# Kernel optimization log

Measured on AMD Instinct MI355X. Metric: run time of the kernel, lower is better.

The kernel has to match this reference:

```python
import jax, jax.numpy as jnp
import numpy as np

B, S, D, H = 4, 4096, 512, 2
PD = D // H  # projection_dim = 256


def setup_inputs() -> dict:
    key = jax.random.key(0)
    ks = jax.random.split(key, 6)
    scale = 1.0 / np.sqrt(D)
    return {
        "x": jax.random.normal(ks[0], (B, S, D), dtype=jnp.float32),
        "Wq": jax.random.normal(ks[1], (D, D), dtype=jnp.float32) * scale,
        "bq": jnp.zeros((D,), dtype=jnp.float32),
        "Wk": jax.random.normal(ks[2], (D, D), dtype=jnp.float32) * scale,
        "bk": jnp.zeros((D,), dtype=jnp.float32),
        "Wv": jax.random.normal(ks[3], (D, D), dtype=jnp.float32) * scale,
        "bv": jnp.zeros((D,), dtype=jnp.float32),
        "Wo": jax.random.normal(ks[4], (D, D), dtype=jnp.float32) * scale,
        "bo": jnp.zeros((D,), dtype=jnp.float32),
    }


def _split_heads(t):
    # [B, S, D] -> [B, H, S, PD]
    return t.reshape(B, S, H, PD).transpose(0, 2, 1, 3)


def reference(x, Wq, bq, Wk, bk, Wv, bv, Wo, bo):
    Q = _split_heads(x @ Wq + bq)
    K = _split_heads(x @ Wk + bk)
    V = _split_heads(x @ Wv + bv)
    # scaled dot-product attention, non-causal (no mask in original)
    scores = jnp.einsum("bhqd,bhkd->bhqk", Q, K) / jnp.sqrt(jnp.float32(PD))
    weights = jax.nn.softmax(scores, axis=-1)
    attn = jnp.einsum("bhqk,bhkd->bhqd", weights, V)
    # merge heads: [B, H, S, PD] -> [B, S, D]
    concat = attn.transpose(0, 2, 1, 3).reshape(B, S, D)
    return concat @ Wo + bo
```

## Files before the change

### kernel.cpp

```cpp
#include <hip/hip_runtime.h>
#include <hip/hip_bf16.h>


#define B_  4
#define S_  4096
#define D_  512
#define H_  2
#define PD_ 256

typedef __attribute__((ext_vector_type(4))) float f32x4;
typedef __attribute__((ext_vector_type(16))) float f32x16;
typedef __attribute__((ext_vector_type(8))) short short8;
typedef __attribute__((ext_vector_type(4))) short short4v;
typedef __attribute__((ext_vector_type(4))) unsigned u32x4;

static __device__ __forceinline__ short f2bf(float f) {
  unsigned u = __float_as_uint(f);
  u += 0x7fffu + ((u >> 16) & 1u);
  return (short)(u >> 16);
}
static __device__ __forceinline__ unsigned pack2(float a, float b) {
  return (unsigned)(unsigned short)f2bf(a) | ((unsigned)(unsigned short)f2bf(b) << 16);
}
static __device__ __forceinline__ void gload16(const short* g, short* l) {
  __builtin_amdgcn_global_load_lds((const __attribute__((address_space(1))) void*)g,
                                   (__attribute__((address_space(3))) void*)l,
                                   16, 0, 0);
}

__global__ void convert_x_kernel(const float* __restrict__ x, short* __restrict__ xb, int n8) {
  int i = blockIdx.x * blockDim.x + threadIdx.x;
  int stride = gridDim.x * blockDim.x;
  for (; i < n8; i += stride) {
    const f32x4* p = (const f32x4*)(x + (size_t)i * 8);
    f32x4 a = p[0], b = p[1];
    short8 v;
    v[0] = f2bf(a[0]); v[1] = f2bf(a[1]); v[2] = f2bf(a[2]); v[3] = f2bf(a[3]);
    v[4] = f2bf(b[0]); v[5] = f2bf(b[1]); v[6] = f2bf(b[2]); v[7] = f2bf(b[3]);
    *(short8*)(xb + (size_t)i * 8) = v;
  }
}

__global__ __launch_bounds__(256) void transpose_w(
    const float* __restrict__ W0, const float* __restrict__ W1,
    const float* __restrict__ W2, const float* __restrict__ W3,
    short* __restrict__ T0, short* __restrict__ T1,
    short* __restrict__ T2, short* __restrict__ T3) {
  const float* W = (blockIdx.z == 0) ? W0 : (blockIdx.z == 1) ? W1 : (blockIdx.z == 2) ? W2 : W3;
  short* T = (blockIdx.z == 0) ? T0 : (blockIdx.z == 1) ? T1 : (blockIdx.z == 2) ? T2 : T3;
  __shared__ float tile[32][33];
  int tx = threadIdx.x & 31, ty = threadIdx.x >> 5;
  int r0 = blockIdx.x * 32, c0 = blockIdx.y * 32;
#pragma unroll
  for (int i = 0; i < 4; ++i)
    tile[ty + 8 * i][tx] = W[(size_t)(r0 + ty + 8 * i) * D_ + c0 + tx];
  __syncthreads();
#pragma unroll
  for (int i = 0; i < 4; ++i)
    T[(size_t)(c0 + ty + 8 * i) * D_ + r0 + tx] = f2bf(tile[tx][ty + 8 * i]);
}

__global__ __launch_bounds__(256) void transpose_v(
    const short* __restrict__ Vw, short* __restrict__ Vt) {
  __shared__ short tile[64][68];
  int h = blockIdx.z;
  int s0 = blockIdx.x * 64, d0 = blockIdx.y * 64;
  const short* src = Vw + (size_t)h * S_ * PD_;
  short* dst = Vt + (size_t)h * S_ * PD_;
  int tx = threadIdx.x & 15, ty = threadIdx.x >> 4;
#pragma unroll
  for (int i = 0; i < 4; ++i) {
    short4v v = *(const short4v*)(src + (size_t)(s0 + ty + 16 * i) * PD_ + d0 + tx * 4);
    *(short4v*)&tile[ty + 16 * i][tx * 4] = v;
  }
  __syncthreads();
#pragma unroll
  for (int i = 0; i < 4; ++i) {
    int d = d0 + ty + 16 * i;
    short4v v;
#pragma unroll
    for (int j = 0; j < 4; ++j) v[j] = tile[tx * 4 + j][ty + 16 * i];
    int swz = (tx >> 1) ^ (d & 7);
    *(short4v*)(dst + (size_t)d * S_ + s0 + (tx & 1) * 4 + swz * 8) = v;
  }
}

template <int MODE>
__global__ __launch_bounds__(256, 2) void gemm_bt(
    const short* __restrict__ A,
    const short* __restrict__ Bt0, const short* __restrict__ Bt1, const short* __restrict__ Bt2,
    const float* __restrict__ b0, const float* __restrict__ b1, const float* __restrict__ b2,
    short* __restrict__ o0, short* __restrict__ o1, short* __restrict__ o2,
    float* __restrict__ fout) {
  __shared__ short sA[128 * 72];
  __shared__ short sB[128 * 72];

  const int tid = threadIdx.x;
  const int lane = tid & 63, wid = tid >> 6;
  const int wr = wid >> 1, wc = wid & 1;
  const int l15 = lane & 15, g = lane >> 4;
  const int m0 = blockIdx.x * 128, n0 = blockIdx.y * 128;

  const short* Bt = (MODE == 0) ? ((blockIdx.z == 0) ? Bt0 : (blockIdx.z == 1) ? Bt1 : Bt2) : Bt0;
  const float* bias = (MODE == 0) ? ((blockIdx.z == 0) ? b0 : (blockIdx.z == 1) ? b1 : b2) : b0;

  short8 pa[4], pb[4];

  auto loadT = [&](int kt) {
#pragma unroll
    for (int i = 0; i < 4; ++i) {
      int slot = tid + 256 * i;
      int r = slot >> 3, gg = slot & 7;
      pa[i] = *(const short8*)(A + (size_t)(m0 + r) * D_ + kt * 64 + 8 * gg);
      pb[i] = *(const short8*)(Bt + (size_t)(n0 + r) * D_ + kt * 64 + 8 * gg);
    }
  };
  auto storeT = [&]() {
#pragma unroll
    for (int i = 0; i < 4; ++i) {
      int slot = tid + 256 * i;
      int r = slot >> 3, gg = slot & 7;
      *(short8*)&sA[r * 72 + 8 * gg] = pa[i];
      *(short8*)&sB[r * 72 + 8 * gg] = pb[i];
    }
  };

  f32x4 acc[4][4];
#pragma unroll
  for (int i = 0; i < 4; ++i)
#pragma unroll
    for (int j = 0; j < 4; ++j) acc[i][j] = (f32x4)0.0f;

  loadT(0);
#pragma unroll 1
  for (int kt = 0; kt < 8; ++kt) {
    __syncthreads();
    storeT();
    if (kt < 7) loadT(kt + 1);
    __syncthreads();
#pragma unroll
    for (int s = 0; s < 2; ++s) {
      short8 a[4], b[4];
#pragma unroll
      for (int fr = 0; fr < 4; ++fr)
        a[fr] = *(const short8*)&sA[(wr * 64 + fr * 16 + l15) * 72 + 32 * s + 8 * g];
#pragma unroll
      for (int fc = 0; fc < 4; ++fc)
        b[fc] = *(const short8*)&sB[(wc * 64 + fc * 16 + l15) * 72 + 32 * s + 8 * g];
#pragma unroll
      for (int fr = 0; fr < 4; ++fr)
#pragma unroll
        for (int fc = 0; fc < 4; ++fc)
          acc[fr][fc] = __builtin_amdgcn_mfma_f32_16x16x32_bf16(a[fr], b[fc], acc[fr][fc], 0, 0, 0);
    }
  }

  if (MODE == 0) {
    short* dst = (blockIdx.z == 0) ? o0 : (blockIdx.z == 1) ? o1 : o2;
    const bool kswz = (blockIdx.z == 1);
#pragma unroll
    for (int fc = 0; fc < 4; ++fc) {
      int n = n0 + wc * 64 + fc * 16 + l15;
      float bvv = bias[n];
      int h = n >> 8, pd = n & 255;
#pragma unroll
      for (int fr = 0; fr < 4; ++fr)
#pragma unroll
        for (int r = 0; r < 4; ++r) {
          int m = m0 + wr * 64 + fr * 16 + 4 * g + r;
          int bb = m >> 12, ss = m & 4095;
          int pdw = pd;
          if (kswz) {
            int ch = pd >> 3;
            pdw = (pd & 7) | (((ch & 24) | ((ch & 7) ^ (ss & 7))) << 3);
          }
          dst[((size_t)((bb * H_ + h) * S_ + ss)) * PD_ + pdw] = f2bf(acc[fr][fc][r] + bvv);
        }
    }
  } else {
#pragma unroll
    for (int fc = 0; fc < 4; ++fc) {
      int n = n0 + wc * 64 + fc * 16 + l15;
      float bvv = bias[n];
#pragma unroll
      for (int fr = 0; fr < 4; ++fr)
#pragma unroll
        for (int r = 0; r < 4; ++r) {
          int m = m0 + wr * 64 + fr * 16 + 4 * g + r;
          fout[(size_t)m * D_ + n] = acc[fr][fc][r] + bvv;
        }
    }
  }
}

__global__ __launch_bounds__(256, 1) void attn2_kernel(
    const short* __restrict__ Qw, const short* __restrict__ Kw,
    const short* __restrict__ Vt, short* __restrict__ ATT) {
  __shared__ short sK[2][64 * 256];
  __shared__ short sV[2][256 * 64];
  __shared__ float sR[4][32];

  const int tid  = threadIdx.x;
  const int lane = tid & 63;
  const int w    = tid >> 6;
  const int l31  = lane & 31;
  const int hi   = lane >> 5;
  const int head = blockIdx.x & 7, qt = blockIdx.x >> 3;
  const size_t hoff = (size_t)head * S_ * PD_;
  const short* Qh = Qw + hoff;
  const short* Kh = Kw + hoff;
  const short* Vh = Vt + hoff;
  const int wbase = tid & ~63;

  const int qrow = qt * 128 + w * 32 + l31;
  short8 qf[16];
#pragma unroll
  for (int dc = 0; dc < 16; ++dc)
    qf[dc] = *(const short8*)(Qh + (size_t)qrow * PD_ + dc * 16 + hi * 8);

  f32x16 o[8];
#pragma unroll
  for (int i = 0; i < 8; ++i) o[i] = (f32x16)0.0f;
  float mrun = -3.0e38f, lrun = 0.0f;

  auto stage = [&](int buf, int t) {
    const short* kp = Kh + (size_t)t * 64 * PD_;
#pragma unroll
    for (int i = 0; i < 8; ++i) {
      int slot = tid + 256 * i;
      gload16(kp + (slot >> 5) * PD_ + (slot & 31) * 8, &sK[buf][(wbase + 256 * i) * 8]);
    }
    const short* vp = Vh + t * 64;
#pragma unroll
    for (int i = 0; i < 8; ++i) {
      int slot = tid + 256 * i;
      gload16(vp + (size_t)(slot >> 3) * S_ + (slot & 7) * 8, &sV[buf][(wbase + 256 * i) * 8]);
    }
  };

  stage(0, 0);
  const int NT = S_ / 64;
#pragma unroll 1
  for (int t = 0; t < NT; ++t) {
    __syncthreads();
    const int buf = t & 1;
    if (t + 1 < NT) stage(buf ^ 1, t + 1);

    f32x16 sacc[2];
    sacc[0] = (f32x16)0.0f; sacc[1] = (f32x16)0.0f;
#pragma unroll
    for (int dc = 0; dc < 16; ++dc) {
      int ch = (2 * dc + hi) ^ (l31 & 7);
      short8 kf0 = *(const short8*)&sK[buf][l31 * 256 + ch * 8];
      sacc[0] = __builtin_amdgcn_mfma_f32_32x32x16_bf16(kf0, qf[dc], sacc[0], 0, 0, 0);
      short8 kf1 = *(const short8*)&sK[buf][(32 + l31) * 256 + ch * 8];
      sacc[1] = __builtin_amdgcn_mfma_f32_32x32x16_bf16(kf1, qf[dc], sacc[1], 0, 0, 0);
    }

    float tmax = sacc[0][0];
#pragma unroll
    for (int r = 1; r < 16; ++r) tmax = fmaxf(tmax, sacc[0][r]);
#pragma unroll
    for (int r = 0; r < 16; ++r) tmax = fmaxf(tmax, sacc[1][r]);
    tmax = fmaxf(tmax, __shfl_xor(tmax, 32));
    const bool skip = __all(tmax <= mrun);
    if (!skip) {
      float mn = fmaxf(mrun, tmax);
      float resc = __expf((mrun - mn) * 0.0625f);
      mrun = mn;
      lrun *= resc;
      if (!hi) sR[w][l31] = resc;
      asm volatile("" ::: "memory");
      f32x4 rv0 = *(const f32x4*)&sR[w][0 + hi * 4];
      f32x4 rv1 = *(const f32x4*)&sR[w][8 + hi * 4];
      f32x4 rv2 = *(const f32x4*)&sR[w][16 + hi * 4];
      f32x4 rv3 = *(const f32x4*)&sR[w][24 + hi * 4];
#pragma unroll
      for (int dcb = 0; dcb < 8; ++dcb)
#pragma unroll
        for (int r = 0; r < 16; ++r) {
          float rr = (r < 4 ? rv0 : r < 8 ? rv1 : r < 12 ? rv2 : rv3)[r & 3];
          o[dcb][r] *= rr;
        }
    }
    float lsum = 0.0f;
#pragma unroll
    for (int kb = 0; kb < 2; ++kb)
#pragma unroll
      for (int r = 0; r < 16; ++r) {
        float p = __expf((sacc[kb][r] - mrun) * 0.0625f);
        sacc[kb][r] = p;
        lsum += p;
      }
    lsum += __shfl_xor(lsum, 32);
    lrun += lsum;

#pragma unroll
    for (int kb = 0; kb < 2; ++kb)
#pragma unroll
      for (int c = 0; c < 2; ++c) {
        unsigned pk0 = pack2(sacc[kb][8 * c + 0], sacc[kb][8 * c + 1]);
        unsigned pk1 = pack2(sacc[kb][8 * c + 2], sacc[kb][8 * c + 3]);
        unsigned pk2 = pack2(sacc[kb][8 * c + 4], sacc[kb][8 * c + 5]);
        unsigned pk3 = pack2(sacc[kb][8 * c + 6], sacc[kb][8 * c + 7]);
        unsigned sh0 = __shfl_xor(pk0, 32);
        unsigned sh1 = __shfl_xor(pk1, 32);
        unsigned sh2 = __shfl_xor(pk2, 32);
        unsigned sh3 = __shfl_xor(pk3, 32);
        u32x4 ua;
        ua[0] = hi ? sh2 : pk0;
        ua[1] = hi ? sh3 : pk1;
        ua[2] = hi ? pk2 : sh0;
        ua[3] = hi ? pk3 : sh1;
        short8 af = *(short8*)&ua;
        const int kc = kb * 2 + c;
#pragma unroll
        for (int dcb = 0; dcb < 8; ++dcb) {
          int d = dcb * 32 + l31;
          int ch = (2 * kc + hi) ^ (d & 7);
          short8 vf = *(const short8*)&sV[buf][d * 64 + ch * 8];
          o[dcb] = __builtin_amdgcn_mfma_f32_32x32x16_bf16(af, vf, o[dcb], 0, 0, 0);
        }
      }
  }

  if (!hi) sR[w][l31] = 1.0f / lrun;
  asm volatile("" ::: "memory");
  f32x4 iv0 = *(const f32x4*)&sR[w][0 + hi * 4];
  f32x4 iv1 = *(const f32x4*)&sR[w][8 + hi * 4];
  f32x4 iv2 = *(const f32x4*)&sR[w][16 + hi * 4];
  f32x4 iv3 = *(const f32x4*)&sR[w][24 + hi * 4];
  const int bb = head >> 1, hh = head & 1;
#pragma unroll
  for (int r = 0; r < 16; ++r) {
    int q = qt * 128 + w * 32 + (r & 3) + 8 * (r >> 2) + 4 * hi;
    float iv = (r < 4 ? iv0 : r < 8 ? iv1 : r < 12 ? iv2 : iv3)[r & 3];
    size_t base = ((size_t)(bb * S_ + q)) * D_ + hh * PD_;
#pragma unroll
    for (int dcb = 0; dcb < 8; ++dcb)
      ATT[base + dcb * 32 + l31] = f2bf(o[dcb][r] * iv);
  }
}

extern "C" void kernel_launch(void* const* d_in, const int* in_sizes, int n_in,
                              void* d_out, int out_size, void* d_ws, size_t ws_size,
                              hipStream_t stream) {
  const float* x  = (const float*)d_in[0];
  const float* Wq = (const float*)d_in[1];
  const float* bq = (const float*)d_in[2];
  const float* Wk = (const float*)d_in[3];
  const float* bk = (const float*)d_in[4];
  const float* Wv = (const float*)d_in[5];
  const float* bv = (const float*)d_in[6];
  const float* Wo = (const float*)d_in[7];
  const float* bo = (const float*)d_in[8];
  float* out = (float*)d_out;

  char* ws = (char*)d_ws;
  const size_t WSZ = (size_t)D_ * D_ * 2;
  const size_t QSZ = (size_t)B_ * H_ * S_ * PD_ * 2;
  short* wtq = (short*)(ws);
  short* wtk = (short*)(ws + WSZ);
  short* wtv = (short*)(ws + 2 * WSZ);
  short* wto = (short*)(ws + 3 * WSZ);
  short* Qw  = (short*)(ws + 4 * WSZ);
  short* Kw  = (short*)(ws + 4 * WSZ + QSZ);
  short* Vw  = (short*)(ws + 4 * WSZ + 2 * QSZ);
  short* ATT = (short*)(ws + 4 * WSZ + 3 * QSZ);
  short* XB  = ATT;
  short* Vtp = (short*)d_out;

  convert_x_kernel<<<dim3(2048), dim3(256), 0, stream>>>(x, XB, (B_ * S_ * D_) / 8);
  transpose_w<<<dim3(16, 16, 4), dim3(256), 0, stream>>>(Wq, Wk, Wv, Wo, wtq, wtk, wtv, wto);
  gemm_bt<0><<<dim3(128, 4, 3), dim3(256), 0, stream>>>(
      XB, wtq, wtk, wtv, bq, bk, bv, Qw, Kw, Vw, (float*)nullptr);
  transpose_v<<<dim3(64, 4, 8), dim3(256), 0, stream>>>(Vw, Vtp);
  attn2_kernel<<<dim3(256), dim3(256), 0, stream>>>(Qw, Kw, Vtp, ATT);
  gemm_bt<1><<<dim3(128, 4, 1), dim3(256), 0, stream>>>(
      ATT, wto, wto, wto, bo, bo, bo, nullptr, nullptr, nullptr, out);
}
```

Baseline: 304.6 us.

## Split attention KV range across warp pairs with 64-query blocks and merge

```diff
diff --git a/kernel.cpp b/kernel.cpp
--- a/kernel.cpp
+++ b/kernel.cpp
@@ -7,6 +7,7 @@
 #define D_  512
 #define H_  2
 #define PD_ 256
+#define SC2 0.09016844f
 
 typedef __attribute__((ext_vector_type(4))) float f32x4;
 typedef __attribute__((ext_vector_type(16))) float f32x16;
@@ -80,8 +81,8 @@
     short4v v;
 #pragma unroll
     for (int j = 0; j < 4; ++j) v[j] = tile[tx * 4 + j][ty + 16 * i];
-    int swz = (tx >> 1) ^ (d & 7);
-    *(short4v*)(dst + (size_t)d * S_ + s0 + (tx & 1) * 4 + swz * 8) = v;
+    int swz = ((tx >> 1) & 3) ^ ((d >> 1) & 3);
+    *(short4v*)(dst + (size_t)d * S_ + s0 + (tx >> 3) * 32 + swz * 8 + (tx & 1) * 4) = v;
   }
 }
 
@@ -193,26 +194,33 @@
   }
 }
 
-__global__ __launch_bounds__(256, 1) void attn2_kernel(
+__global__ __launch_bounds__(256, 2) void attn3_kernel(
     const short* __restrict__ Qw, const short* __restrict__ Kw,
     const short* __restrict__ Vt, short* __restrict__ ATT) {
-  __shared__ short sK[2][64 * 256];
-  __shared__ short sV[2][256 * 64];
-  __shared__ float sR[4][32];
-
-  const int tid  = threadIdx.x;
-  const int lane = tid & 63;
-  const int w    = tid >> 6;
-  const int l31  = lane & 31;
-  const int hi   = lane >> 5;
-  const int head = blockIdx.x & 7, qt = blockIdx.x >> 3;
+  __shared__ __align__(16) char smem[66560];
+  __shared__ float sB1[4][32];
+  __shared__ float sMm[4][32];
+  __shared__ float sMl[2][32];
+  short* sK0 = (short*)smem;
+  short* sK1 = (short*)(smem + 16384);
+  short* sV0 = (short*)(smem + 32768);
+  short* sV1 = (short*)(smem + 49152);
+
+  const int tid = threadIdx.x, lane = tid & 63, w = tid >> 6;
+  const int l31 = lane & 31, hi = lane >> 5;
+  const int head = blockIdx.x & 7, qb = blockIdx.x >> 3;
   const size_t hoff = (size_t)head * S_ * PD_;
   const short* Qh = Qw + hoff;
   const short* Kh = Kw + hoff;
   const short* Vh = Vt + hoff;
   const int wbase = tid & ~63;
-
-  const int qrow = qt * 128 + w * 32 + l31;
+  const int kh = w >> 1;
+  const int kbase = kh * 2048;
+
+  short* sKh = kh ? sK1 : sK0;
+  short* sVh = kh ? sV1 : sV0;
+
+  const int qrow = qb * 64 + (w & 1) * 32 + l31;
   short8 qf[16];
 #pragma unroll
   for (int dc = 0; dc < 16; ++dc)
@@ -223,58 +231,53 @@
   for (int i = 0; i < 8; ++i) o[i] = (f32x16)0.0f;
   float mrun = -3.0e38f, lrun = 0.0f;
 
-  auto stage = [&](int buf, int t) {
-    const short* kp = Kh + (size_t)t * 64 * PD_;
-#pragma unroll
-    for (int i = 0; i < 8; ++i) {
-      int slot = tid + 256 * i;
-      gload16(kp + (slot >> 5) * PD_ + (slot & 31) * 8, &sK[buf][(wbase + 256 * i) * 8]);
-    }
-    const short* vp = Vh + t * 64;
-#pragma unroll
-    for (int i = 0; i < 8; ++i) {
-      int slot = tid + 256 * i;
-      gload16(vp + (size_t)(slot >> 3) * S_ + (slot & 7) * 8, &sV[buf][(wbase + 256 * i) * 8]);
+  auto stage = [&](int t) {
+    const int k0 = t * 32;
+#pragma unroll
+    for (int i = 0; i < 4; ++i) {
+      int s = tid + 256 * i;
+      short* ldst = (short*)((char*)nullptr);
+      (void)ldst;
+      gload16(Kh + (size_t)(k0 + (s >> 5)) * PD_ + (s & 31) * 8,
+              sK0 + (size_t)(wbase + 256 * i) * 8);
+      gload16(Kh + (size_t)(2048 + k0 + (s >> 5)) * PD_ + (s & 31) * 8,
+              sK1 + (size_t)(wbase + 256 * i) * 8);
+      gload16(Vh + (size_t)(s >> 2) * S_ + k0 + (s & 3) * 8,
+              sV0 + (size_t)(wbase + 256 * i) * 8);
+      gload16(Vh + (size_t)(s >> 2) * S_ + 2048 + k0 + (s & 3) * 8,
+              sV1 + (size_t)(wbase + 256 * i) * 8);
     }
   };
 
-  stage(0, 0);
-  const int NT = S_ / 64;
 #pragma unroll 1
-  for (int t = 0; t < NT; ++t) {
+  for (int t = 0; t < 64; ++t) {
     __syncthreads();
-    const int buf = t & 1;
-    if (t + 1 < NT) stage(buf ^ 1, t + 1);
-
-    f32x16 sacc[2];
-    sacc[0] = (f32x16)0.0f; sacc[1] = (f32x16)0.0f;
+    stage(t);
+    __syncthreads();
+
+    f32x16 sacc = (f32x16)0.0f;
 #pragma unroll
     for (int dc = 0; dc < 16; ++dc) {
       int ch = (2 * dc + hi) ^ (l31 & 7);
-      short8 kf0 = *(const short8*)&sK[buf][l31 * 256 + ch * 8];
-      sacc[0] = __builtin_amdgcn_mfma_f32_32x32x16_bf16(kf0, qf[dc], sacc[0], 0, 0, 0);
-      short8 kf1 = *(const short8*)&sK[buf][(32 + l31) * 256 + ch * 8];
-      sacc[1] = __builtin_amdgcn_mfma_f32_32x32x16_bf16(kf1, qf[dc], sacc[1], 0, 0, 0);
-    }
-
-    float tmax = sacc[0][0];
-#pragma unroll
-    for (int r = 1; r < 16; ++r) tmax = fmaxf(tmax, sacc[0][r]);
-#pragma unroll
-    for (int r = 0; r < 16; ++r) tmax = fmaxf(tmax, sacc[1][r]);
+      short8 kf = *(const short8*)&sKh[l31 * 256 + ch * 8];
+      sacc = __builtin_amdgcn_mfma_f32_32x32x16_bf16(kf, qf[dc], sacc, 0, 0, 0);
+    }
+
+    float tmax = sacc[0];
+#pragma unroll
+    for (int r = 1; r < 16; ++r) tmax = fmaxf(tmax, sacc[r]);
     tmax = fmaxf(tmax, __shfl_xor(tmax, 32));
-    const bool skip = __all(tmax <= mrun);
-    if (!skip) {
+    if (!__all(tmax <= mrun + 16.0f)) {
       float mn = fmaxf(mrun, tmax);
-      float resc = __expf((mrun - mn) * 0.0625f);
+      float resc = exp2f((mrun - mn) * SC2);
       mrun = mn;
       lrun *= resc;
-      if (!hi) sR[w][l31] = resc;
+      if (!hi) sB1[w][l31] = resc;
       asm volatile("" ::: "memory");
-      f32x4 rv0 = *(const f32x4*)&sR[w][0 + hi * 4];
-      f32x4 rv1 = *(const f32x4*)&sR[w][8 + hi * 4];
-      f32x4 rv2 = *(const f32x4*)&sR[w][16 + hi * 4];
-      f32x4 rv3 = *(const f32x4*)&sR[w][24 + hi * 4];
+      f32x4 rv0 = *(const f32x4*)&sB1[w][0 + hi * 4];
+      f32x4 rv1 = *(const f32x4*)&sB1[w][8 + hi * 4];
+      f32x4 rv2 = *(const f32x4*)&sB1[w][16 + hi * 4];
+      f32x4 rv3 = *(const f32x4*)&sB1[w][24 + hi * 4];
 #pragma unroll
       for (int dcb = 0; dcb < 8; ++dcb)
 #pragma unroll
@@ -285,60 +288,108 @@
     }
     float lsum = 0.0f;
 #pragma unroll
-    for (int kb = 0; kb < 2; ++kb)
-#pragma unroll
-      for (int r = 0; r < 16; ++r) {
-        float p = __expf((sacc[kb][r] - mrun) * 0.0625f);
-        sacc[kb][r] = p;
-        lsum += p;
-      }
+    for (int r = 0; r < 16; ++r) {
+      float p = exp2f((sacc[r] - mrun) * SC2);
+      sacc[r] = p;
+      lsum += p;
+    }
     lsum += __shfl_xor(lsum, 32);
     lrun += lsum;
 
 #pragma unroll
-    for (int kb = 0; kb < 2; ++kb)
-#pragma unroll
-      for (int c = 0; c < 2; ++c) {
-        unsigned pk0 = pack2(sacc[kb][8 * c + 0], sacc[kb][8 * c + 1]);
-        unsigned pk1 = pack2(sacc[kb][8 * c + 2], sacc[kb][8 * c + 3]);
-        unsigned pk2 = pack2(sacc[kb][8 * c + 4], sacc[kb][8 * c + 5]);
-        unsigned pk3 = pack2(sacc[kb][8 * c + 6], sacc[kb][8 * c + 7]);
-        unsigned sh0 = __shfl_xor(pk0, 32);
-        unsigned sh1 = __shfl_xor(pk1, 32);
-        unsigned sh2 = __shfl_xor(pk2, 32);
-        unsigned sh3 = __shfl_xor(pk3, 32);
-        u32x4 ua;
-        ua[0] = hi ? sh2 : pk0;
-        ua[1] = hi ? sh3 : pk1;
-        ua[2] = hi ? pk2 : sh0;
-        ua[3] = hi ? pk3 : sh1;
-        short8 af = *(short8*)&ua;
-        const int kc = kb * 2 + c;
-#pragma unroll
-        for (int dcb = 0; dcb < 8; ++dcb) {
-          int d = dcb * 32 + l31;
-          int ch = (2 * kc + hi) ^ (d & 7);
-          short8 vf = *(const short8*)&sV[buf][d * 64 + ch * 8];
-          o[dcb] = __builtin_amdgcn_mfma_f32_32x32x16_bf16(af, vf, o[dcb], 0, 0, 0);
-        }
+    for (int c = 0; c < 2; ++c) {
+      unsigned pk0 = pack2(sacc[8 * c + 0], sacc[8 * c + 1]);
+      unsigned pk1 = pack2(sacc[8 * c + 2], sacc[8 * c + 3]);
+      unsigned pk2 = pack2(sacc[8 * c + 4], sacc[8 * c + 5]);
+      unsigned pk3 = pack2(sacc[8 * c + 6], sacc[8 * c + 7]);
+      unsigned sh0 = __shfl_xor(pk0, 32);
+      unsigned sh1 = __shfl_xor(pk1, 32);
+      unsigned sh2 = __shfl_xor(pk2, 32);
+      unsigned sh3 = __shfl_xor(pk3, 32);
+      u32x4 ua;
+      ua[0] = hi ? sh2 : pk0;
+      ua[1] = hi ? sh3 : pk1;
+      ua[2] = hi ? pk2 : sh0;
+      ua[3] = hi ? pk3 : sh1;
+      short8 af = *(short8*)&ua;
+      const int ch = (2 * c + hi) ^ ((l31 >> 1) & 3);
+#pragma unroll
+      for (int dcb = 0; dcb < 8; ++dcb) {
+        short8 vf = *(const short8*)&sVh[(size_t)(dcb * 32 + l31) * 32 + ch * 8];
+        o[dcb] = __builtin_amdgcn_mfma_f32_32x32x16_bf16(af, vf, o[dcb], 0, 0, 0);
       }
-  }
-
-  if (!hi) sR[w][l31] = 1.0f / lrun;
-  asm volatile("" ::: "memory");
-  f32x4 iv0 = *(const f32x4*)&sR[w][0 + hi * 4];
-  f32x4 iv1 = *(const f32x4*)&sR[w][8 + hi * 4];
-  f32x4 iv2 = *(const f32x4*)&sR[w][16 + hi * 4];
-  f32x4 iv3 = *(const f32x4*)&sR[w][24 + hi * 4];
-  const int bb = head >> 1, hh = head & 1;
-#pragma unroll
-  for (int r = 0; r < 16; ++r) {
-    int q = qt * 128 + w * 32 + (r & 3) + 8 * (r >> 2) + 4 * hi;
-    float iv = (r < 4 ? iv0 : r < 8 ? iv1 : r < 12 ? iv2 : iv3)[r & 3];
-    size_t base = ((size_t)(bb * S_ + q)) * D_ + hh * PD_;
+    }
+  }
+
+  __syncthreads();
+  if (!hi) sMm[w][l31] = mrun;
+  __syncthreads();
+  {
+    float mo = sMm[w ^ 2][l31];
+    float mf = fmaxf(mrun, mo);
+    float sc = exp2f((mrun - mf) * SC2);
+    lrun *= sc;
+    if (!hi) sB1[w][l31] = sc;
+    asm volatile("" ::: "memory");
+    f32x4 rv0 = *(const f32x4*)&sB1[w][0 + hi * 4];
+    f32x4 rv1 = *(const f32x4*)&sB1[w][8 + hi * 4];
+    f32x4 rv2 = *(const f32x4*)&sB1[w][16 + hi * 4];
+    f32x4 rv3 = *(const f32x4*)&sB1[w][24 + hi * 4];
 #pragma unroll
     for (int dcb = 0; dcb < 8; ++dcb)
-      ATT[base + dcb * 32 + l31] = f2bf(o[dcb][r] * iv);
+#pragma unroll
+      for (int r = 0; r < 16; ++r) {
+        float rr = (r < 4 ? rv0 : r < 8 ? rv1 : r < 12 ? rv2 : rv3)[r & 3];
+        o[dcb][r] *= rr;
+      }
+    if (w >= 2 && !hi) sMl[w - 2][l31] = lrun;
+  }
+  __syncthreads();
+  float* mb = (float*)smem;
+  if (w >= 2) {
+    float* rg = mb + (size_t)(w - 2) * 8320;
+#pragma unroll
+    for (int dcb = 0; dcb < 8; ++dcb)
+#pragma unroll
+      for (int r4 = 0; r4 < 4; ++r4) {
+        f32x4 v;
+        v[0] = o[dcb][4 * r4 + 0];
+        v[1] = o[dcb][4 * r4 + 1];
+        v[2] = o[dcb][4 * r4 + 2];
+        v[3] = o[dcb][4 * r4 + 3];
+        *(f32x4*)&rg[(size_t)(dcb * 4 + r4) * 260 + lane * 4] = v;
+      }
+  }
+  __syncthreads();
+  if (w < 2) {
+    float* rg = mb + (size_t)w * 8320;
+#pragma unroll
+    for (int dcb = 0; dcb < 8; ++dcb)
+#pragma unroll
+      for (int r4 = 0; r4 < 4; ++r4) {
+        f32x4 v = *(const f32x4*)&rg[(size_t)(dcb * 4 + r4) * 260 + lane * 4];
+        o[dcb][4 * r4 + 0] += v[0];
+        o[dcb][4 * r4 + 1] += v[1];
+        o[dcb][4 * r4 + 2] += v[2];
+        o[dcb][4 * r4 + 3] += v[3];
+      }
+    lrun += sMl[w][l31];
+    if (!hi) sB1[w][l31] = 1.0f / lrun;
+    asm volatile("" ::: "memory");
+    f32x4 iv0 = *(const f32x4*)&sB1[w][0 + hi * 4];
+    f32x4 iv1 = *(const f32x4*)&sB1[w][8 + hi * 4];
+    f32x4 iv2 = *(const f32x4*)&sB1[w][16 + hi * 4];
+    f32x4 iv3 = *(const f32x4*)&sB1[w][24 + hi * 4];
+    const int bb = head >> 1, hh = head & 1;
+#pragma unroll
+    for (int r = 0; r < 16; ++r) {
+      int q = qb * 64 + (w & 1) * 32 + (r & 3) + 8 * (r >> 2) + 4 * hi;
+      float iv = (r < 4 ? iv0 : r < 8 ? iv1 : r < 12 ? iv2 : iv3)[r & 3];
+      size_t base = ((size_t)(bb * S_ + q)) * D_ + hh * PD_;
+#pragma unroll
+      for (int dcb = 0; dcb < 8; ++dcb)
+        ATT[base + dcb * 32 + l31] = f2bf(o[dcb][r] * iv);
+    }
   }
 }
 
@@ -375,7 +426,7 @@
   gemm_bt<0><<<dim3(128, 4, 3), dim3(256), 0, stream>>>(
       XB, wtq, wtk, wtv, bq, bk, bv, Qw, Kw, Vw, (float*)nullptr);
   transpose_v<<<dim3(64, 4, 8), dim3(256), 0, stream>>>(Vw, Vtp);
-  attn2_kernel<<<dim3(256), dim3(256), 0, stream>>>(Qw, Kw, Vtp, ATT);
+  attn3_kernel<<<dim3(512), dim3(256), 0, stream>>>(Qw, Kw, Vtp, ATT);
   gemm_bt<1><<<dim3(128, 4, 1), dim3(256), 0, stream>>>(
       ATT, wto, wto, wto, bo, bo, bo, nullptr, nullptr, nullptr, out);
 }
```

New measurement: 292.6 us. -3.9%, faster.

## Split attention keys across two wave groups and read K/V directly from global

Applied to the files above, without the earlier changes.

```diff
diff --git a/kernel.cpp b/kernel.cpp
--- a/kernel.cpp
+++ b/kernel.cpp
@@ -7,6 +7,7 @@
 #define D_  512
 #define H_  2
 #define PD_ 256
+#define QSCALE 0.09016844f
 
 typedef __attribute__((ext_vector_type(4))) float f32x4;
 typedef __attribute__((ext_vector_type(16))) float f32x16;
@@ -19,13 +20,10 @@
   u += 0x7fffu + ((u >> 16) & 1u);
   return (short)(u >> 16);
 }
-static __device__ __forceinline__ unsigned pack2(float a, float b) {
-  return (unsigned)(unsigned short)f2bf(a) | ((unsigned)(unsigned short)f2bf(b) << 16);
-}
-static __device__ __forceinline__ void gload16(const short* g, short* l) {
-  __builtin_amdgcn_global_load_lds((const __attribute__((address_space(1))) void*)g,
-                                   (__attribute__((address_space(3))) void*)l,
-                                   16, 0, 0);
+static __device__ __forceinline__ unsigned cvtpk(float a, float b) {
+  unsigned r;
+  asm("v_cvt_pk_bf16_f32 %0, %1, %2" : "=v"(r) : "v"(a), "v"(b));
+  return r;
 }
 
 __global__ void convert_x_kernel(const float* __restrict__ x, short* __restrict__ xb, int n8) {
@@ -80,8 +78,7 @@
     short4v v;
 #pragma unroll
     for (int j = 0; j < 4; ++j) v[j] = tile[tx * 4 + j][ty + 16 * i];
-    int swz = (tx >> 1) ^ (d & 7);
-    *(short4v*)(dst + (size_t)d * S_ + s0 + (tx & 1) * 4 + swz * 8) = v;
+    *(short4v*)(dst + (size_t)d * S_ + s0 + tx * 4) = v;
   }
 }
 
@@ -157,7 +154,7 @@
 
   if (MODE == 0) {
     short* dst = (blockIdx.z == 0) ? o0 : (blockIdx.z == 1) ? o1 : o2;
-    const bool kswz = (blockIdx.z == 1);
+    const float sc = (blockIdx.z == 0) ? QSCALE : 1.0f;
 #pragma unroll
     for (int fc = 0; fc < 4; ++fc) {
       int n = n0 + wc * 64 + fc * 16 + l15;
@@ -169,12 +166,7 @@
         for (int r = 0; r < 4; ++r) {
           int m = m0 + wr * 64 + fr * 16 + 4 * g + r;
           int bb = m >> 12, ss = m & 4095;
-          int pdw = pd;
-          if (kswz) {
-            int ch = pd >> 3;
-            pdw = (pd & 7) | (((ch & 24) | ((ch & 7) ^ (ss & 7))) << 3);
-          }
-          dst[((size_t)((bb * H_ + h) * S_ + ss)) * PD_ + pdw] = f2bf(acc[fr][fc][r] + bvv);
+          dst[((size_t)((bb * H_ + h) * S_ + ss)) * PD_ + pd] = f2bf((acc[fr][fc][r] + bvv) * sc);
         }
     }
   } else {
@@ -193,152 +185,161 @@
   }
 }
 
-__global__ __launch_bounds__(256, 1) void attn2_kernel(
+__global__ __launch_bounds__(512, 2) void attn10_kernel(
     const short* __restrict__ Qw, const short* __restrict__ Kw,
     const short* __restrict__ Vt, short* __restrict__ ATT) {
-  __shared__ short sK[2][64 * 256];
-  __shared__ short sV[2][256 * 64];
-  __shared__ float sR[4][32];
-
-  const int tid  = threadIdx.x;
-  const int lane = tid & 63;
-  const int w    = tid >> 6;
-  const int l31  = lane & 31;
-  const int hi   = lane >> 5;
-  const int head = blockIdx.x & 7, qt = blockIdx.x >> 3;
+  __shared__ __align__(16) char smem[137216];
+
+  const int tid = threadIdx.x, lane = tid & 63, w = tid >> 6;
+  const int l31 = lane & 31, hi = lane >> 5;
+  const int head = blockIdx.x & 7, qb = blockIdx.x >> 3;
+  const int kh = w >> 2, qg = w & 3;
   const size_t hoff = (size_t)head * S_ * PD_;
   const short* Qh = Qw + hoff;
-  const short* Kh = Kw + hoff;
-  const short* Vh = Vt + hoff;
-  const int wbase = tid & ~63;
-
-  const int qrow = qt * 128 + w * 32 + l31;
+
+  const int qrow = qb * 128 + qg * 32 + l31;
   short8 qf[16];
 #pragma unroll
   for (int dc = 0; dc < 16; ++dc)
     qf[dc] = *(const short8*)(Qh + (size_t)qrow * PD_ + dc * 16 + hi * 8);
 
+  const short* kp = Kw + hoff + (size_t)(kh * 2048 + l31) * PD_ + hi * 8;
+  const short* vp = Vt + hoff + (size_t)l31 * S_ + kh * 2048 + hi * 8;
+
   f32x16 o[8];
 #pragma unroll
   for (int i = 0; i < 8; ++i) o[i] = (f32x16)0.0f;
   float mrun = -3.0e38f, lrun = 0.0f;
 
-  auto stage = [&](int buf, int t) {
-    const short* kp = Kh + (size_t)t * 64 * PD_;
-#pragma unroll
-    for (int i = 0; i < 8; ++i) {
-      int slot = tid + 256 * i;
-      gload16(kp + (slot >> 5) * PD_ + (slot & 31) * 8, &sK[buf][(wbase + 256 * i) * 8]);
-    }
-    const short* vp = Vh + t * 64;
-#pragma unroll
-    for (int i = 0; i < 8; ++i) {
-      int slot = tid + 256 * i;
-      gload16(vp + (size_t)(slot >> 3) * S_ + (slot & 7) * 8, &sV[buf][(wbase + 256 * i) * 8]);
-    }
-  };
-
-  stage(0, 0);
-  const int NT = S_ / 64;
 #pragma unroll 1
-  for (int t = 0; t < NT; ++t) {
-    __syncthreads();
-    const int buf = t & 1;
-    if (t + 1 < NT) stage(buf ^ 1, t + 1);
-
-    f32x16 sacc[2];
-    sacc[0] = (f32x16)0.0f; sacc[1] = (f32x16)0.0f;
-#pragma unroll
-    for (int dc = 0; dc < 16; ++dc) {
-      int ch = (2 * dc + hi) ^ (l31 & 7);
-      short8 kf0 = *(const short8*)&sK[buf][l31 * 256 + ch * 8];
-      sacc[0] = __builtin_amdgcn_mfma_f32_32x32x16_bf16(kf0, qf[dc], sacc[0], 0, 0, 0);
-      short8 kf1 = *(const short8*)&sK[buf][(32 + l31) * 256 + ch * 8];
-      sacc[1] = __builtin_amdgcn_mfma_f32_32x32x16_bf16(kf1, qf[dc], sacc[1], 0, 0, 0);
-    }
-
-    float tmax = sacc[0][0];
-#pragma unroll
-    for (int r = 1; r < 16; ++r) tmax = fmaxf(tmax, sacc[0][r]);
-#pragma unroll
-    for (int r = 0; r < 16; ++r) tmax = fmaxf(tmax, sacc[1][r]);
-    tmax = fmaxf(tmax, __shfl_xor(tmax, 32));
-    const bool skip = __all(tmax <= mrun);
-    if (!skip) {
-      float mn = fmaxf(mrun, tmax);
-      float resc = __expf((mrun - mn) * 0.0625f);
-      mrun = mn;
-      lrun *= resc;
-      if (!hi) sR[w][l31] = resc;
-      asm volatile("" ::: "memory");
-      f32x4 rv0 = *(const f32x4*)&sR[w][0 + hi * 4];
-      f32x4 rv1 = *(const f32x4*)&sR[w][8 + hi * 4];
-      f32x4 rv2 = *(const f32x4*)&sR[w][16 + hi * 4];
-      f32x4 rv3 = *(const f32x4*)&sR[w][24 + hi * 4];
-#pragma unroll
-      for (int dcb = 0; dcb < 8; ++dcb)
+  for (int t = 0; t < 64; ++t) {
+    __builtin_amdgcn_s_barrier();
+
+    f32x16 _a = (f32x16)0.0f, _b = (f32x16)0.0f;
+#pragma unroll
+    for (int a2 = 0; a2 < 4; ++a2)
+#pragma unroll
+      for (int b2 = 0; b2 < 4; ++b2) {
+        short8 kf = *(const short8*)(kp + (4 * a2 + b2) * 16);
+        if (b2 & 1)
+          _b = __builtin_amdgcn_mfma_f32_32x32x16_bf16(kf, qf[4 * a2 + b2], _b, 0, 0, 0);
+        else
+          _a = __builtin_amdgcn_mfma_f32_32x32x16_bf16(kf, qf[4 * a2 + b2], _a, 0, 0, 0);
+      }
+    f32x16 sS = _a + _b;
+    kp += 32 * PD_;
+
+    {
+      float t0 = fmaxf(sS[0], sS[1]),   t1 = fmaxf(sS[2], sS[3]);
+      float t2 = fmaxf(sS[4], sS[5]),   t3 = fmaxf(sS[6], sS[7]);
+      float t4 = fmaxf(sS[8], sS[9]),   t5 = fmaxf(sS[10], sS[11]);
+      float t6 = fmaxf(sS[12], sS[13]), t7 = fmaxf(sS[14], sS[15]);
+      t0 = fmaxf(t0, t1); t2 = fmaxf(t2, t3); t4 = fmaxf(t4, t5); t6 = fmaxf(t6, t7);
+      t0 = fmaxf(t0, t2); t4 = fmaxf(t4, t6);
+      float tmax = fmaxf(t0, t4);
+      tmax = fmaxf(tmax, __shfl_xor(tmax, 32));
+      if (!__all(tmax <= mrun + 8.0f)) {
+        float mn = fmaxf(mrun, tmax);
+        float resc = exp2f(mrun - mn);
+        mrun = mn; lrun *= resc;
 #pragma unroll
         for (int r = 0; r < 16; ++r) {
-          float rr = (r < 4 ? rv0 : r < 8 ? rv1 : r < 12 ? rv2 : rv3)[r & 3];
-          o[dcb][r] *= rr;
+          float rr = __shfl(resc, (r & 3) + 8 * (r >> 2) + 4 * hi, 64);
+#pragma unroll
+          for (int d = 0; d < 8; ++d) o[d][r] *= rr;
         }
-    }
-    float lsum = 0.0f;
-#pragma unroll
-    for (int kb = 0; kb < 2; ++kb)
-#pragma unroll
-      for (int r = 0; r < 16; ++r) {
-        float p = __expf((sacc[kb][r] - mrun) * 0.0625f);
-        sacc[kb][r] = p;
-        lsum += p;
-      }
-    lsum += __shfl_xor(lsum, 32);
-    lrun += lsum;
-
-#pragma unroll
-    for (int kb = 0; kb < 2; ++kb)
-#pragma unroll
-      for (int c = 0; c < 2; ++c) {
-        unsigned pk0 = pack2(sacc[kb][8 * c + 0], sacc[kb][8 * c + 1]);
-        unsigned pk1 = pack2(sacc[kb][8 * c + 2], sacc[kb][8 * c + 3]);
-        unsigned pk2 = pack2(sacc[kb][8 * c + 4], sacc[kb][8 * c + 5]);
-        unsigned pk3 = pack2(sacc[kb][8 * c + 6], sacc[kb][8 * c + 7]);
-        unsigned sh0 = __shfl_xor(pk0, 32);
-        unsigned sh1 = __shfl_xor(pk1, 32);
-        unsigned sh2 = __shfl_xor(pk2, 32);
-        unsigned sh3 = __shfl_xor(pk3, 32);
-        u32x4 ua;
-        ua[0] = hi ? sh2 : pk0;
-        ua[1] = hi ? sh3 : pk1;
-        ua[2] = hi ? pk2 : sh0;
-        ua[3] = hi ? pk3 : sh1;
-        short8 af = *(short8*)&ua;
-        const int kc = kb * 2 + c;
-#pragma unroll
-        for (int dcb = 0; dcb < 8; ++dcb) {
-          int d = dcb * 32 + l31;
-          int ch = (2 * kc + hi) ^ (d & 7);
-          short8 vf = *(const short8*)&sV[buf][d * 64 + ch * 8];
-          o[dcb] = __builtin_amdgcn_mfma_f32_32x32x16_bf16(af, vf, o[dcb], 0, 0, 0);
-        }
-      }
-  }
-
-  if (!hi) sR[w][l31] = 1.0f / lrun;
-  asm volatile("" ::: "memory");
-  f32x4 iv0 = *(const f32x4*)&sR[w][0 + hi * 4];
-  f32x4 iv1 = *(const f32x4*)&sR[w][8 + hi * 4];
-  f32x4 iv2 = *(const f32x4*)&sR[w][16 + hi * 4];
-  f32x4 iv3 = *(const f32x4*)&sR[w][24 + hi * 4];
-  const int bb = head >> 1, hh = head & 1;
-#pragma unroll
-  for (int r = 0; r < 16; ++r) {
-    int q = qt * 128 + w * 32 + (r & 3) + 8 * (r >> 2) + 4 * hi;
-    float iv = (r < 4 ? iv0 : r < 8 ? iv1 : r < 12 ? iv2 : iv3)[r & 3];
-    size_t base = ((size_t)(bb * S_ + q)) * D_ + hh * PD_;
-#pragma unroll
-    for (int dcb = 0; dcb < 8; ++dcb)
-      ATT[base + dcb * 32 + l31] = f2bf(o[dcb][r] * iv);
+      }
+#pragma unroll
+      for (int r = 0; r < 16; ++r) sS[r] = exp2f(sS[r] - mrun);
+      float u0 = (sS[0] + sS[1]) + (sS[2] + sS[3]);
+      float u1 = (sS[4] + sS[5]) + (sS[6] + sS[7]);
+      u0 += (sS[8] + sS[9]) + (sS[10] + sS[11]);
+      u1 += (sS[12] + sS[13]) + (sS[14] + sS[15]);
+      float ls = u0 + u1;
+      ls += __shfl_xor(ls, 32);
+      lrun += ls;
+    }
+
+#pragma unroll
+    for (int c = 0; c < 2; ++c) {
+      unsigned pk0 = cvtpk(sS[8 * c + 0], sS[8 * c + 1]);
+      unsigned pk1 = cvtpk(sS[8 * c + 2], sS[8 * c + 3]);
+      unsigned pk2 = cvtpk(sS[8 * c + 4], sS[8 * c + 5]);
+      unsigned pk3 = cvtpk(sS[8 * c + 6], sS[8 * c + 7]);
+      unsigned sh0 = __shfl_xor(pk0, 32);
+      unsigned sh1 = __shfl_xor(pk1, 32);
+      unsigned sh2 = __shfl_xor(pk2, 32);
+      unsigned sh3 = __shfl_xor(pk3, 32);
+      u32x4 ua;
+      ua[0] = hi ? sh2 : pk0;
+      ua[1] = hi ? sh3 : pk1;
+      ua[2] = hi ? pk2 : sh0;
+      ua[3] = hi ? pk3 : sh1;
+      short8 af = *(short8*)&ua;
+#pragma unroll
+      for (int dcb = 0; dcb < 8; ++dcb) {
+        short8 vf = *(const short8*)(vp + (size_t)dcb * 32 * S_ + c * 16);
+        o[dcb] = __builtin_amdgcn_mfma_f32_32x32x16_bf16(af, vf, o[dcb], 0, 0, 0);
+      }
+    }
+    vp += 32;
+  }
+
+  __syncthreads();
+  float* sMm = (float*)smem;
+  float* sMl = (float*)(smem + 1024);
+  float* dep = (float*)(smem + 4096);
+  if (!hi) sMm[w * 32 + l31] = mrun;
+  __syncthreads();
+  {
+    float mo = sMm[(w ^ 4) * 32 + l31];
+    float mf = fmaxf(mrun, mo);
+    float sc = exp2f(mrun - mf);
+    lrun *= sc;
+#pragma unroll
+    for (int r = 0; r < 16; ++r) {
+      float rr = __shfl(sc, (r & 3) + 8 * (r >> 2) + 4 * hi, 64);
+#pragma unroll
+      for (int d = 0; d < 8; ++d) o[d][r] *= rr;
+    }
+    if (w >= 4 && !hi) sMl[(w - 4) * 32 + l31] = lrun;
+  }
+  __syncthreads();
+  if (w >= 4) {
+    float* rg = dep + (size_t)qg * 8320;
+#pragma unroll
+    for (int d = 0; d < 8; ++d)
+#pragma unroll
+      for (int r4 = 0; r4 < 4; ++r4) {
+        f32x4 v;
+#pragma unroll
+        for (int j = 0; j < 4; ++j) v[j] = o[d][4 * r4 + j];
+        *(f32x4*)&rg[(size_t)(d * 4 + r4) * 260 + lane * 4] = v;
+      }
+  }
+  __syncthreads();
+  if (w < 4) {
+    float* rg = dep + (size_t)qg * 8320;
+#pragma unroll
+    for (int d = 0; d < 8; ++d)
+#pragma unroll
+      for (int r4 = 0; r4 < 4; ++r4) {
+        f32x4 v = *(const f32x4*)&rg[(size_t)(d * 4 + r4) * 260 + lane * 4];
+#pragma unroll
+        for (int j = 0; j < 4; ++j) o[d][4 * r4 + j] += v[j];
+      }
+    lrun += sMl[qg * 32 + l31];
+    float inv = 1.0f / lrun;
+    const int bb = head >> 1, hh = head & 1;
+#pragma unroll
+    for (int r = 0; r < 16; ++r) {
+      int q = qb * 128 + qg * 32 + (r & 3) + 8 * (r >> 2) + 4 * hi;
+      float iv = __shfl(inv, (r & 3) + 8 * (r >> 2) + 4 * hi, 64);
+      size_t base = ((size_t)(bb * S_ + q)) * D_ + hh * PD_;
+#pragma unroll
+      for (int d = 0; d < 8; ++d)
+        ATT[base + d * 32 + l31] = f2bf(o[d][r] * iv);
+    }
   }
 }
 
@@ -375,7 +376,7 @@
   gemm_bt<0><<<dim3(128, 4, 3), dim3(256), 0, stream>>>(
       XB, wtq, wtk, wtv, bq, bk, bv, Qw, Kw, Vw, (float*)nullptr);
   transpose_v<<<dim3(64, 4, 8), dim3(256), 0, stream>>>(Vw, Vtp);
-  attn2_kernel<<<dim3(256), dim3(256), 0, stream>>>(Qw, Kw, Vtp, ATT);
+  attn10_kernel<<<dim3(256), dim3(512), 0, stream>>>(Qw, Kw, Vtp, ATT);
   gemm_bt<1><<<dim3(128, 4, 1), dim3(256), 0, stream>>>(
       ATT, wto, wto, wto, bo, bo, bo, nullptr, nullptr, nullptr, out);
 }
```

Result: slower. 626.2 us (+105.6%).
